# Optimization experiments

Hardware: AMD Instinct MI355X
Metric: run time of the kernel (lower is better)

The kernel has to match this reference:

```python
import jax, jax.numpy as jnp
import numpy as np

H = 256
N = 64           # d_state; diagonal SSM uses N//2 conjugate-pair modes
N2 = N // 2
B, L = 16, 4096
EPS = 1e-5


def layernorm(x, g, b):
    m = jnp.mean(x, axis=-1, keepdims=True)
    v = jnp.mean((x - m) ** 2, axis=-1, keepdims=True)
    return (x - m) / jnp.sqrt(v + EPS) * g + b


def s4_layer(u, log_dt, A_re, A_im, C_re, C_im, D, Wout, bout):
    # u: (B, L, H). Bidirectional diagonal S4 (S4D-style ZOH kernel), channels=1.
    Bb, Ll, Hh = u.shape
    dt = jnp.exp(log_dt)                       # (H,)
    A = A_re + 1j * A_im                       # (H, N2), Re(A) < 0
    dtA = dt[:, None] * A                      # (H, N2)
    # ZOH discretization folded into C:  C <- C * (exp(dtA) - 1) / A
    C = (C_re + 1j * C_im) * (jnp.exp(dtA) - 1.0) / A   # (2, H, N2)
    vand = jnp.exp(dtA[:, :, None] * jnp.arange(Ll))    # (H, N2, L)
    k = 2.0 * jnp.einsum('chn,hnl->chl', C, vand).real  # (2, H, L)
    k_fwd, k_bwd = k[0], k[1]
    # bidirectional: causal kernel + anticausal (flipped, shifted by L)
    z = jnp.zeros_like(k_fwd)
    k2 = jnp.concatenate([k_fwd, z], axis=-1) \
       + jnp.concatenate([z, k_bwd[:, ::-1]], axis=-1)  # (H, 2L)
    ut = jnp.transpose(u, (0, 2, 1))                    # (B, H, L)
    n_fft = 2 * Ll
    y = jnp.fft.irfft(jnp.fft.rfft(ut, n=n_fft) * jnp.fft.rfft(k2, n=n_fft), n=n_fft)[..., :Ll]
    y = y + ut * D[:, None]                             # skip connection
    y = jax.nn.gelu(y, approximate=False)
    y = jnp.transpose(y, (0, 2, 1))                     # (B, L, H)
    zz = y @ Wout + bout                                # (B, L, 2H)
    return zz[..., :Hh] * jax.nn.sigmoid(zz[..., Hh:])  # GLU output projection


def setup_inputs() -> dict:
    key = jax.random.key(0)
    ks = jax.random.split(key, 16)
    x = jax.random.normal(ks[0], (B, L, H), dtype=jnp.float32)
    log_dt = jnp.log(0.001) + jax.random.uniform(ks[1], (H,)) * (jnp.log(0.1) - jnp.log(0.001))
    A_re = -0.5 * jnp.ones((H, N2), dtype=jnp.float32)
    A_im = jnp.pi * jnp.broadcast_to(jnp.arange(N2, dtype=jnp.float32), (H, N2))
    C_re = jax.random.normal(ks[2], (2, H, N2), dtype=jnp.float32) * 0.5
    C_im = jax.random.normal(ks[3], (2, H, N2), dtype=jnp.float32) * 0.5
    Dskip = jax.random.normal(ks[4], (H,), dtype=jnp.float32)
    Wout = jax.random.normal(ks[5], (H, 2 * H), dtype=jnp.float32) / np.sqrt(H)
    bout = jnp.zeros((2 * H,), dtype=jnp.float32)
    ln1_g = jnp.ones((H,), jnp.float32); ln1_b = jnp.zeros((H,), jnp.float32)
    ln2_g = jnp.ones((H,), jnp.float32); ln2_b = jnp.zeros((H,), jnp.float32)
    W2 = jax.random.normal(ks[6], (H, 2 * H), dtype=jnp.float32) / np.sqrt(H)
    b2 = jnp.zeros((2 * H,), jnp.float32)
    W3 = jax.random.normal(ks[7], (2 * H, H), dtype=jnp.float32) / np.sqrt(2 * H)
    b3 = jnp.zeros((H,), jnp.float32)
    return dict(x=x, ln1_g=ln1_g, ln1_b=ln1_b, ln2_g=ln2_g, ln2_b=ln2_b,
                log_dt=log_dt, A_re=A_re, A_im=A_im, C_re=C_re, C_im=C_im,
                Dskip=Dskip, Wout=Wout, bout=bout, W2=W2, b2=b2, W3=W3, b3=b3)


def reference(x, ln1_g, ln1_b, ln2_g, ln2_b, log_dt, A_re, A_im, C_re, C_im,
              Dskip, Wout, bout, W2, b2, W3, b3):
    # residual S4 sub-block
    y = x
    h = layernorm(x, ln1_g, ln1_b)
    h = s4_layer(h, log_dt, A_re, A_im, C_re, C_im, Dskip, Wout, bout)
    x = y + h
    # residual MLP sub-block
    y = x
    h = layernorm(x, ln2_g, ln2_b)
    h = jax.nn.gelu(h @ W2 + b2, approximate=False)
    h = h @ W3 + b3
    return y + h
```

## Files before the change

### kernel.cpp

```cpp
#include <hip/hip_runtime.h>
#include <hip/hip_bf16.h>

typedef __attribute__((ext_vector_type(8))) short bf16x8;
typedef __attribute__((ext_vector_type(4))) float f32x4;

#define Hdim 256
#define NM 32
#define NB 16
#define LL 4096
#define PCH 256
#define NCH 16
#define KBIG 384

#define OFF_ABIG ((size_t)0)
#define OFF_WPM  ((size_t)50331648)
#define OFF_UT   ((size_t)67108864)
#define OFF_ZG   ((size_t)100663296)
#define OFF_M    ((size_t)67108864)
#define OFF_ZP   ((size_t)134217728)
#define OFF_G    ((size_t)150994944)
#define OFF_WTAB ((size_t)185073664)
#define OFF_WPT  ((size_t)185139200)
#define OFF_CE   ((size_t)185204736)
#define OFF_W1T  ((size_t)185335808)
#define OFF_W2T  ((size_t)185597952)
#define OFF_W3T  ((size_t)185860096)

typedef const __attribute__((address_space(1))) void* gas_p;
typedef __attribute__((address_space(3))) void* las_p;

__device__ __forceinline__ float gelu_f(float v) {
    float u = 0.7978845608028654f * fmaf(0.044715f * v * v, v, v);
    float uc = fminf(fmaxf(u, -15.f), 15.f);
    float e = __expf(2.f * uc);
    return 0.5f * v * (1.f + (e - 1.f) * __builtin_amdgcn_rcpf(e + 1.f));
}
__device__ __forceinline__ unsigned short f2bf(float f) {
    unsigned int u = __float_as_uint(f);
    u += 0x7fffu + ((u >> 16) & 1u);
    return (unsigned short)(u >> 16);
}
__device__ __forceinline__ float bf2f(unsigned short u) {
    return __uint_as_float((unsigned int)u << 16);
}

__device__ __forceinline__ bf16x8 fr(const unsigned short* lds, int row, int kcol) {
    return *(const bf16x8*)(lds + row * 64 + ((((kcol >> 3) ^ (row & 7)) << 3)));
}

template<int ROWS, int THREADS>
__device__ __forceinline__ void stage64(const unsigned short* __restrict__ src, int ld, int k0,
                                        unsigned short* lds, int t) {
    constexpr int EPI = THREADS * 8;
#pragma unroll
    for (int i = 0; i < (ROWS * 64) / EPI; i++) {
        int e = i * EPI + t * 8;
        int r = e >> 6;
        int k = (((e >> 3) & 7) ^ (r & 7)) << 3;
        const unsigned short* g = src + (size_t)r * ld + (k0 + k);
        unsigned short* l = lds + i * EPI + (t >> 6) * 512;
        __builtin_amdgcn_global_load_lds((gas_p)g, (las_p)l, 16, 0, 0);
    }
}

template<int ROWS, int THREADS>
__device__ __forceinline__ void stageUT(const unsigned short* __restrict__ UT, int h, int rbase,
                                        int k0, unsigned short* lds, int t) {
    constexpr int EPI = THREADS * 8;
#pragma unroll
    for (int i = 0; i < (ROWS * 64) / EPI; i++) {
        int e = i * EPI + t * 8;
        int r = e >> 6;
        int k = (((e >> 3) & 7) ^ (r & 7)) << 3;
        int row = rbase + r;
        const unsigned short* g = UT + ((size_t)((row >> 4) * Hdim + h)) * LL
                                  + (row & 15) * PCH + (k0 + k);
        unsigned short* l = lds + i * EPI + (t >> 6) * 512;
        __builtin_amdgcn_global_load_lds((gas_p)g, (las_p)l, 16, 0, 0);
    }
}

__global__ void k_tab(const float* __restrict__ logdt, const float* __restrict__ Are,
                      const float* __restrict__ Aim, const float* __restrict__ Cre,
                      const float* __restrict__ Cim, float2* __restrict__ wtab,
                      float2* __restrict__ wptab, float2* __restrict__ ceff) {
    int idx = blockIdx.x * blockDim.x + threadIdx.x;
    if (idx >= Hdim * NM) return;
    int h = idx >> 5;
    float dt = expf(logdt[h]);
    double dar = (double)dt * (double)Are[idx];
    double dai = (double)dt * (double)Aim[idx];
    double wm = exp(dar);
    double wr = wm * cos(dai), wi = wm * sin(dai);
    wtab[idx] = make_float2((float)wr, (float)wi);
    double pm = exp(dar * (double)PCH);
    double pai = dai * (double)PCH;
    wptab[idx] = make_float2((float)(pm * cos(pai)), (float)(pm * sin(pai)));
    double are = (double)Are[idx], aim = (double)Aim[idx];
    double den = are * are + aim * aim;
    double nr = wr - 1.0, ni = wi;
    double qr = (nr * are + ni * aim) / den;
    double qi = (ni * are - nr * aim) / den;
    for (int ch = 0; ch < 2; ch++) {
        double cr = (double)Cre[ch * Hdim * NM + idx];
        double ci = (double)Cim[ch * Hdim * NM + idx];
        ceff[ch * Hdim * NM + idx] = make_float2((float)(cr * qr - ci * qi),
                                                 (float)(cr * qi + ci * qr));
    }
}

__global__ void k_wt(const float* __restrict__ W1, const float* __restrict__ W2,
                     const float* __restrict__ W3, unsigned short* __restrict__ W1T,
                     unsigned short* __restrict__ W2T, unsigned short* __restrict__ W3T) {
    int t = blockIdx.x * 256 + threadIdx.x;
    int k = t >> 9, n = t & 511;
    W1T[n * 256 + k] = f2bf(W1[t]);
    W2T[n * 256 + k] = f2bf(W2[t]);
    int k3 = t >> 8, n3 = t & 255;
    W3T[n3 * 512 + k3] = f2bf(W3[t]);
}

__global__ __launch_bounds__(256) void k_abw(const float* __restrict__ logdt,
                                             const float* __restrict__ Are,
                                             const float* __restrict__ Aim,
                                             const float2* __restrict__ CE,
                                             const float* __restrict__ Dsk,
                                             unsigned short* __restrict__ AB,
                                             unsigned short* __restrict__ Wp) {
    __shared__ float2 wpow[32][257];
    __shared__ float kf[256], kb[256];
    __shared__ float2 ce_s[64];
    int h = blockIdx.x;
    int part = blockIdx.y;
    int t = threadIdx.x;
    if (t < 64) ce_s[t] = CE[(t >> 5) * (Hdim * NM) + h * NM + (t & 31)];
    {
        int n = t >> 3, seg = t & 7;
        float dt = expf(logdt[h]);
        float dar = dt * Are[h * NM + n], dai = dt * Aim[h * NM + n];
        float em = expf(dar);
        float wr = em * cosf(dai), wi = em * sinf(dai);
        int j0 = seg * 32;
        float m = expf((float)j0 * dar), ang = (float)j0 * dai;
        float vr = m * cosf(ang), vi = m * sinf(ang);
        for (int q = 0; q < 32; q++) {
            wpow[n][j0 + q] = make_float2(vr, vi);
            float nr2 = vr * wr - vi * wi;
            float ni2 = vr * wi + vi * wr;
            vr = nr2; vi = ni2;
        }
        if (seg == 7) wpow[n][256] = make_float2(vr, vi);
    }
    __syncthreads();
    if (part == 4) {
        for (int r = 0; r < 128; r++) {
            int n = (r & 63) >> 1, reim = r & 1, dir = r >> 6;
            float2 wv = wpow[n][dir ? t : 255 - t];
            Wp[((size_t)h * 128 + r) * 256 + t] = f2bf(reim ? wv.y : wv.x);
        }
        return;
    }
    {
        float kfv = 0.f, kbv = 0.f;
#pragma unroll
        for (int n = 0; n < NM; n++) {
            float2 wv = wpow[n][t];
            float2 cf = ce_s[n], cb = ce_s[32 + n];
            kfv = fmaf(cf.x, wv.x, fmaf(-cf.y, wv.y, kfv));
            kbv = fmaf(cb.x, wv.x, fmaf(-cb.y, wv.y, kbv));
        }
        kf[t] = 2.f * kfv;
        kb[t] = 2.f * kbv;
    }
    __syncthreads();
    float dsk = Dsk[h];
    int j0 = part * 64;
    for (int j = j0; j < j0 + 64; j++) {
        unsigned short* out = AB + ((size_t)h * 256 + j) * KBIG;
        float v = (t <= j) ? kf[j - t] : kb[t - j - 1];
        if (t == j) v += dsk;
        out[t] = f2bf(v);
        if (t < 128) {
            int n = (t & 63) >> 1, reim = t & 1;
            float2 c = (t < 64) ? ce_s[n] : ce_s[32 + n];
            float2 wv = (t < 64) ? wpow[n][j + 1] : wpow[n][255 - j];
            float re = c.x * wv.x - c.y * wv.y;
            float im = c.x * wv.y + c.y * wv.x;
            out[256 + t] = f2bf(reim ? -2.f * im : 2.f * re);
        }
    }
}

__global__ __launch_bounds__(256) void k_lntr(const float* __restrict__ x,
                                              const float* __restrict__ g,
                                              const float* __restrict__ bt,
                                              unsigned short* __restrict__ UT) {
    __shared__ unsigned short lds[256][65];
    int lt = blockIdx.x, b = blockIdx.y;
    int t = threadIdx.x;
    int lane = t & 63, w = t >> 6;
    float4 gg = ((const float4*)g)[lane];
    float4 bb = ((const float4*)bt)[lane];
#pragma unroll
    for (int q = 0; q < 16; q++) {
        int l = q * 4 + w;
        float4 v = ((const float4*)(x + ((size_t)(b * LL + lt * 64 + l)) * Hdim))[lane];
        float s = v.x + v.y + v.z + v.w;
        float ss = v.x * v.x + v.y * v.y + v.z * v.z + v.w * v.w;
#pragma unroll
        for (int o = 1; o < 64; o <<= 1) { s += __shfl_xor(s, o, 64); ss += __shfl_xor(ss, o, 64); }
        float mean = s * (1.0f / Hdim);
        float var = ss * (1.0f / Hdim) - mean * mean;
        float rstd = rsqrtf(var + 1e-5f);
        lds[lane * 4 + 0][l] = f2bf((v.x - mean) * rstd * gg.x + bb.x);
        lds[lane * 4 + 1][l] = f2bf((v.y - mean) * rstd * gg.y + bb.y);
        lds[lane * 4 + 2][l] = f2bf((v.z - mean) * rstd * gg.z + bb.z);
        lds[lane * 4 + 3][l] = f2bf((v.w - mean) * rstd * gg.w + bb.w);
    }
    __syncthreads();
    for (int q = 0; q < 64; q++) {
        int idx = q * 256 + t;
        int hh = idx >> 6, ll = idx & 63;
        UT[((size_t)(b * Hdim + hh)) * LL + lt * 64 + ll] = lds[hh][ll];
    }
}

__global__ void k_ln_bf(const unsigned short* __restrict__ x, const float* __restrict__ g,
                        const float* __restrict__ bt, unsigned short* __restrict__ out) {
    int row = blockIdx.x * 4 + (threadIdx.x >> 6);
    int lane = threadIdx.x & 63;
    ushort4 u4 = ((const ushort4*)(x + (size_t)row * Hdim))[lane];
    float vx = bf2f(u4.x), vy = bf2f(u4.y), vz = bf2f(u4.z), vw = bf2f(u4.w);
    float s = vx + vy + vz + vw;
    float ss = vx * vx + vy * vy + vz * vz + vw * vw;
#pragma unroll
    for (int o = 1; o < 64; o <<= 1) { s += __shfl_xor(s, o, 64); ss += __shfl_xor(ss, o, 64); }
    float mean = s * (1.0f / Hdim);
    float var = ss * (1.0f / Hdim) - mean * mean;
    float rstd = rsqrtf(var + 1e-5f);
    float4 gg = ((const float4*)g)[lane];
    float4 bb = ((const float4*)bt)[lane];
    ushort4 o;
    o.x = f2bf((vx - mean) * rstd * gg.x + bb.x);
    o.y = f2bf((vy - mean) * rstd * gg.y + bb.y);
    o.z = f2bf((vz - mean) * rstd * gg.z + bb.z);
    o.w = f2bf((vw - mean) * rstd * gg.w + bb.w);
    ((ushort4*)(out + (size_t)row * Hdim))[lane] = o;
}

__global__ __launch_bounds__(512) void k_zgemm(const unsigned short* __restrict__ UT,
                                               const unsigned short* __restrict__ Wp,
                                               float* __restrict__ Zg) {
    __shared__ unsigned short As[256 * 64];
    __shared__ unsigned short Bs[128 * 64];
    int h = blockIdx.x;
    int t = threadIdx.x;
    int w = t >> 6, lane = t & 63;
    int m0 = (w & 3) * 64;
    int nb = (w >> 2) * 64;
    int lr = lane & 15, lk = (lane >> 4) * 8;
    f32x4 acc[4][4];
#pragma unroll
    for (int i = 0; i < 4; i++)
#pragma unroll
        for (int jx = 0; jx < 4; jx++) acc[i][jx] = (f32x4){0.f, 0.f, 0.f, 0.f};
    for (int k0 = 0; k0 < 256; k0 += 64) {
        stageUT<256, 512>(UT, h, 0, k0, As, t);
        stage64<128, 512>(Wp + (size_t)h * 128 * 256, 256, k0, Bs, t);
        __syncthreads();
#pragma unroll
        for (int kk = 0; kk < 64; kk += 32) {
            bf16x8 a[4], b[4];
#pragma unroll
            for (int mi = 0; mi < 4; mi++) a[mi] = fr(As, m0 + mi * 16 + lr, kk + lk);
#pragma unroll
            for (int nf = 0; nf < 4; nf++) b[nf] = fr(Bs, nb + nf * 16 + lr, kk + lk);
#pragma unroll
            for (int mi = 0; mi < 4; mi++)
#pragma unroll
                for (int nf = 0; nf < 4; nf++)
                    acc[mi][nf] = __builtin_amdgcn_mfma_f32_16x16x32_bf16(a[mi], b[nf], acc[mi][nf], 0, 0, 0);
        }
        __syncthreads();
    }
#pragma unroll
    for (int mi = 0; mi < 4; mi++)
#pragma unroll
        for (int nf = 0; nf < 4; nf++) {
            int col = nb + nf * 16 + lr;
#pragma unroll
            for (int r = 0; r < 4; r++) {
                int row = m0 + mi * 16 + (lane >> 4) * 4 + r;
                Zg[((size_t)h * 256 + row) * 128 + col] = acc[mi][nf][r];
            }
        }
}

__global__ void k_prefix2(const float* __restrict__ Zg, const float2* __restrict__ wptab,
                          unsigned short* __restrict__ ZP) {
    int t = blockIdx.x * 256 + threadIdx.x;
    int n = t & 31;
    int h = (t >> 5) & 255;
    int b = (t >> 13) & 15;
    int dir = (t >> 17) & 1;
    float2 wp = wptab[h * NM + n];
    float sr = 0.f, si = 0.f;
    int ro = dir ? 64 + 2 * n : 2 * n;
    if (dir == 0) {
        for (int c = 0; c < NCH; c++) {
            size_t base = ((size_t)h * 256 + b * NCH + c) * 128;
            ZP[base + ro] = f2bf(sr);
            ZP[base + ro + 1] = f2bf(si);
            float zr = Zg[base + ro], zi = Zg[base + ro + 1];
            float nr = fmaf(wp.x, sr, fmaf(-wp.y, si, zr));
            float ni = fmaf(wp.y, sr, fmaf(wp.x, si, zi));
            sr = nr; si = ni;
        }
    } else {
        for (int c = NCH - 1; c >= 0; c--) {
            size_t base = ((size_t)h * 256 + b * NCH + c) * 128;
            ZP[base + ro] = f2bf(sr);
            ZP[base + ro + 1] = f2bf(si);
            float zr = Zg[base + ro], zi = Zg[base + ro + 1];
            float nr = fmaf(wp.x, sr, fmaf(-wp.y, si, zr));
            float ni = fmaf(wp.y, sr, fmaf(wp.x, si, zi));
            sr = nr; si = ni;
        }
    }
}

__global__ __launch_bounds__(512) void k_conv(const unsigned short* __restrict__ UT,
                                              const unsigned short* __restrict__ ZP,
                                              const unsigned short* __restrict__ AB,
                                              unsigned short* __restrict__ Yt) {
    __shared__ unsigned short As[128 * 64];
    __shared__ unsigned short Bs[256 * 64];
    int wgid = ((int)blockIdx.x % 8) * 64 + (int)blockIdx.x / 8;
    int h = wgid >> 1;
    int mbase = (wgid & 1) * 128;
    int t = threadIdx.x;
    int w = t >> 6, lane = t & 63;
    int m0 = (w & 1) * 64;
    int nb = (w >> 1) * 64;
    int lr = lane & 15, lk = (lane >> 4) * 8;
    const unsigned short* ABh = AB + (size_t)h * 256 * KBIG;
    f32x4 acc[4][4];
#pragma unroll
    for (int i = 0; i < 4; i++)
#pragma unroll
        for (int jx = 0; jx < 4; jx++) acc[i][jx] = (f32x4){0.f, 0.f, 0.f, 0.f};
    for (int k0 = 0; k0 < 256; k0 += 64) {
        stageUT<128, 512>(UT, h, mbase, k0, As, t);
        stage64<256, 512>(ABh, KBIG, k0, Bs, t);
        __syncthreads();
#pragma unroll
        for (int kk = 0; kk < 64; kk += 32) {
            bf16x8 a[4], b[4];
#pragma unroll
            for (int mi = 0; mi < 4; mi++) a[mi] = fr(As, m0 + mi * 16 + lr, kk + lk);
#pragma unroll
            for (int nf = 0; nf < 4; nf++) b[nf] = fr(Bs, nb + nf * 16 + lr, kk + lk);
#pragma unroll
            for (int mi = 0; mi < 4; mi++)
#pragma unroll
                for (int nf = 0; nf < 4; nf++)
                    acc[mi][nf] = __builtin_amdgcn_mfma_f32_16x16x32_bf16(a[mi], b[nf], acc[mi][nf], 0, 0, 0);
        }
        __syncthreads();
    }
    for (int k0 = 0; k0 < 128; k0 += 64) {
        stage64<128, 512>(ZP + ((size_t)h * 256 + mbase) * 128, 128, k0, As, t);
        stage64<256, 512>(ABh + 256, KBIG, k0, Bs, t);
        __syncthreads();
#pragma unroll
        for (int kk = 0; kk < 64; kk += 32) {
            bf16x8 a[4], b[4];
#pragma unroll
            for (int mi = 0; mi < 4; mi++) a[mi] = fr(As, m0 + mi * 16 + lr, kk + lk);
#pragma unroll
            for (int nf = 0; nf < 4; nf++) b[nf] = fr(Bs, nb + nf * 16 + lr, kk + lk);
#pragma unroll
            for (int mi = 0; mi < 4; mi++)
#pragma unroll
                for (int nf = 0; nf < 4; nf++)
                    acc[mi][nf] = __builtin_amdgcn_mfma_f32_16x16x32_bf16(a[mi], b[nf], acc[mi][nf], 0, 0, 0);
        }
        __syncthreads();
    }
#pragma unroll
    for (int mi = 0; mi < 4; mi++)
#pragma unroll
        for (int nf = 0; nf < 4; nf++) {
            int col = nb + nf * 16 + lr;
#pragma unroll
            for (int r = 0; r < 4; r++) {
                int row = mbase + m0 + mi * 16 + (lane >> 4) * 4 + r;
                Yt[(size_t)h * 65536 + row * 256 + col] = f2bf(gelu_f(acc[mi][nf][r]));
            }
        }
}

__global__ void k_trg(const unsigned short* __restrict__ Yt, unsigned short* __restrict__ G) {
    __shared__ unsigned short lds[64][65];
    int bc = blockIdx.x;
    int h0 = blockIdx.y * 64, j0 = blockIdx.z * 64;
    int t = threadIdx.x;
#pragma unroll
    for (int q = 0; q < 16; q++) {
        int idx = q * 256 + t;
        int hh = idx >> 6, jj = idx & 63;
        lds[hh][jj] = Yt[(size_t)(h0 + hh) * 65536 + bc * 256 + j0 + jj];
    }
    __syncthreads();
    int b = bc >> 4, c = bc & 15;
#pragma unroll
    for (int q = 0; q < 16; q++) {
        int idx = q * 256 + t;
        int jj = idx >> 6, hh = idx & 63;
        G[((size_t)(b * LL + c * PCH + j0 + jj)) * Hdim + h0 + hh] = lds[hh][jj];
    }
}

__global__ __launch_bounds__(512) void k_gemm1(const unsigned short* __restrict__ Gm,
                                               const unsigned short* __restrict__ W1T,
                                               const float* __restrict__ bo,
                                               const float* __restrict__ xin,
                                               unsigned short* __restrict__ X2) {
    __shared__ unsigned short As[128 * 64];
    __shared__ unsigned short BsA[128 * 64];
    __shared__ unsigned short BsB[128 * 64];
    int t = threadIdx.x;
    int w = t >> 6, lane = t & 63;
    int m0w = (w & 1) * 64;
    int n0w = (w >> 1) * 32;
    int lr = lane & 15, lk = (lane >> 4) * 8;
    int mblk = blockIdx.x * 128, nblk = blockIdx.y * 128;
    const unsigned short* Ab  = Gm + (size_t)mblk * 256;
    const unsigned short* BbA = W1T + (size_t)nblk * 256;
    const unsigned short* BbB = W1T + (size_t)(nblk + 256) * 256;
    f32x4 acc[4][4];
#pragma unroll
    for (int i = 0; i < 4; i++)
#pragma unroll
        for (int j = 0; j < 4; j++) acc[i][j] = (f32x4){0.f, 0.f, 0.f, 0.f};
    for (int k0 = 0; k0 < 256; k0 += 64) {
        stage64<128, 512>(Ab, 256, k0, As, t);
        stage64<128, 512>(BbA, 256, k0, BsA, t);
        stage64<128, 512>(BbB, 256, k0, BsB, t);
        __syncthreads();
#pragma unroll
        for (int kk = 0; kk < 64; kk += 32) {
            bf16x8 a[4], bA[2], bB[2];
#pragma unroll
            for (int mi = 0; mi < 4; mi++)
                a[mi] = fr(As, m0w + mi * 16 + lr, kk + lk);
#pragma unroll
            for (int nf = 0; nf < 2; nf++) {
                bA[nf] = fr(BsA, n0w + nf * 16 + lr, kk + lk);
                bB[nf] = fr(BsB, n0w + nf * 16 + lr, kk + lk);
            }
#pragma unroll
            for (int mi = 0; mi < 4; mi++)
#pragma unroll
                for (int nf = 0; nf < 2; nf++) {
                    acc[mi][nf] = __builtin_amdgcn_mfma_f32_16x16x32_bf16(a[mi], bA[nf], acc[mi][nf], 0, 0, 0);
                    acc[mi][nf + 2] = __builtin_amdgcn_mfma_f32_16x16x32_bf16(a[mi], bB[nf], acc[mi][nf + 2], 0, 0, 0);
                }
        }
        __syncthreads();
    }
#pragma unroll
    for (int mi = 0; mi < 4; mi++)
#pragma unroll
        for (int nf = 0; nf < 2; nf++) {
            int col = nblk + n0w + nf * 16 + lr;
            float biasA = bo[col], biasB = bo[col + 256];
#pragma unroll
            for (int r = 0; r < 4; r++) {
                int row = mblk + m0w + mi * 16 + (lane >> 4) * 4 + r;
                float zzA = acc[mi][nf][r] + biasA;
                float zzB = acc[mi][nf + 2][r] + biasB;
                float v = zzA * __builtin_amdgcn_rcpf(1.0f + __expf(-zzB));
                size_t idx = (size_t)row * 256 + col;
                X2[idx] = f2bf(xin[idx] + v);
            }
        }
}

__global__ __launch_bounds__(512) void k_gemm2(const unsigned short* __restrict__ T2,
                                               const unsigned short* __restrict__ W2T,
                                               const float* __restrict__ b2,
                                               unsigned short* __restrict__ Mo) {
    __shared__ unsigned short As[128 * 64];
    __shared__ unsigned short Bs[256 * 64];
    int t = threadIdx.x;
    int w = t >> 6, lane = t & 63;
    int m0w = (w & 1) * 64;
    int n0w = (w >> 1) * 64;
    int lr = lane & 15, lk = (lane >> 4) * 8;
    int mblk = blockIdx.x * 128, nblk = blockIdx.y * 256;
    const unsigned short* Ab = T2 + (size_t)mblk * 256;
    const unsigned short* Bb = W2T + (size_t)nblk * 256;
    f32x4 acc[4][4];
#pragma unroll
    for (int i = 0; i < 4; i++)
#pragma unroll
        for (int j = 0; j < 4; j++) acc[i][j] = (f32x4){0.f, 0.f, 0.f, 0.f};
    for (int k0 = 0; k0 < 256; k0 += 64) {
        stage64<128, 512>(Ab, 256, k0, As, t);
        stage64<256, 512>(Bb, 256, k0, Bs, t);
        __syncthreads();
#pragma unroll
        for (int kk = 0; kk < 64; kk += 32) {
            bf16x8 a[4], b[4];
#pragma unroll
            for (int mi = 0; mi < 4; mi++)
                a[mi] = fr(As, m0w + mi * 16 + lr, kk + lk);
#pragma unroll
            for (int nf = 0; nf < 4; nf++)
                b[nf] = fr(Bs, n0w + nf * 16 + lr, kk + lk);
#pragma unroll
            for (int mi = 0; mi < 4; mi++)
#pragma unroll
                for (int nf = 0; nf < 4; nf++)
                    acc[mi][nf] = __builtin_amdgcn_mfma_f32_16x16x32_bf16(a[mi], b[nf], acc[mi][nf], 0, 0, 0);
        }
        __syncthreads();
    }
#pragma unroll
    for (int mi = 0; mi < 4; mi++)
#pragma unroll
        for (int nf = 0; nf < 4; nf++) {
            int col = nblk + n0w + nf * 16 + lr;
            float bias = b2[col];
#pragma unroll
            for (int r = 0; r < 4; r++) {
                int row = mblk + m0w + mi * 16 + (lane >> 4) * 4 + r;
                Mo[(size_t)row * 512 + col] = f2bf(gelu_f(acc[mi][nf][r] + bias));
            }
        }
}

__global__ __launch_bounds__(512) void k_gemm3(const unsigned short* __restrict__ Mb,
                                               const unsigned short* __restrict__ W3T,
                                               const float* __restrict__ b3,
                                               const unsigned short* __restrict__ X2,
                                               float* __restrict__ out) {
    __shared__ unsigned short As[128 * 64];
    __shared__ unsigned short Bs[256 * 64];
    int t = threadIdx.x;
    int w = t >> 6, lane = t & 63;
    int m0w = (w & 1) * 64;
    int n0w = (w >> 1) * 64;
    int lr = lane & 15, lk = (lane >> 4) * 8;
    int mblk = blockIdx.x * 128;
    const unsigned short* Ab = Mb + (size_t)mblk * 512;
    f32x4 acc[4][4];
#pragma unroll
    for (int i = 0; i < 4; i++)
#pragma unroll
        for (int j = 0; j < 4; j++) acc[i][j] = (f32x4){0.f, 0.f, 0.f, 0.f};
    for (int k0 = 0; k0 < 512; k0 += 64) {
        stage64<128, 512>(Ab, 512, k0, As, t);
        stage64<256, 512>(W3T, 512, k0, Bs, t);
        __syncthreads();
#pragma unroll
        for (int kk = 0; kk < 64; kk += 32) {
            bf16x8 a[4], b[4];
#pragma unroll
            for (int mi = 0; mi < 4; mi++)
                a[mi] = fr(As, m0w + mi * 16 + lr, kk + lk);
#pragma unroll
            for (int nf = 0; nf < 4; nf++)
                b[nf] = fr(Bs, n0w + nf * 16 + lr, kk + lk);
#pragma unroll
            for (int mi = 0; mi < 4; mi++)
#pragma unroll
                for (int nf = 0; nf < 4; nf++)
                    acc[mi][nf] = __builtin_amdgcn_mfma_f32_16x16x32_bf16(a[mi], b[nf], acc[mi][nf], 0, 0, 0);
        }
        __syncthreads();
    }
#pragma unroll
    for (int mi = 0; mi < 4; mi++)
#pragma unroll
        for (int nf = 0; nf < 4; nf++) {
            int col = n0w + nf * 16 + lr;
            float bias = b3[col];
#pragma unroll
            for (int r = 0; r < 4; r++) {
                int row = mblk + m0w + mi * 16 + (lane >> 4) * 4 + r;
                size_t idx = (size_t)row * 256 + col;
                out[idx] = bf2f(X2[idx]) + acc[mi][nf][r] + bias;
            }
        }
}

extern "C" void kernel_launch(void* const* d_in, const int* in_sizes, int n_in,
                              void* d_out, int out_size, void* d_ws, size_t ws_size,
                              hipStream_t stream) {
    const float* x     = (const float*)d_in[0];
    const float* ln1g  = (const float*)d_in[1];
    const float* ln1b  = (const float*)d_in[2];
    const float* ln2g  = (const float*)d_in[3];
    const float* ln2b  = (const float*)d_in[4];
    const float* logdt = (const float*)d_in[5];
    const float* Are   = (const float*)d_in[6];
    const float* Aim   = (const float*)d_in[7];
    const float* Cre   = (const float*)d_in[8];
    const float* Cim   = (const float*)d_in[9];
    const float* Dsk   = (const float*)d_in[10];
    const float* Wout  = (const float*)d_in[11];
    const float* bo    = (const float*)d_in[12];
    const float* W2    = (const float*)d_in[13];
    const float* b2    = (const float*)d_in[14];
    const float* W3    = (const float*)d_in[15];
    const float* b3    = (const float*)d_in[16];

    char* ws = (char*)d_ws;
    unsigned short* AB   = (unsigned short*)(ws + OFF_ABIG);
    unsigned short* Wp   = (unsigned short*)(ws + OFF_WPM);
    unsigned short* X2   = (unsigned short*)(ws + OFF_ABIG);
    unsigned short* UT   = (unsigned short*)(ws + OFF_UT);
    float*          Zg   = (float*)(ws + OFF_ZG);
    unsigned short* Yt   = (unsigned short*)(ws + OFF_ZG);
    unsigned short* Mb   = (unsigned short*)(ws + OFF_M);
    unsigned short* ZP   = (unsigned short*)(ws + OFF_ZP);
    unsigned short* G    = (unsigned short*)(ws + OFF_G);
    float2*         WT   = (float2*)(ws + OFF_WTAB);
    float2*         WPT  = (float2*)(ws + OFF_WPT);
    float2*         CE   = (float2*)(ws + OFF_CE);
    unsigned short* W1T  = (unsigned short*)(ws + OFF_W1T);
    unsigned short* W2T  = (unsigned short*)(ws + OFF_W2T);
    unsigned short* W3T  = (unsigned short*)(ws + OFF_W3T);

    k_tab<<<32, 256, 0, stream>>>(logdt, Are, Aim, Cre, Cim, WT, WPT, CE);
    k_wt<<<512, 256, 0, stream>>>(Wout, W2, W3, W1T, W2T, W3T);
    k_lntr<<<dim3(64, 16), 256, 0, stream>>>(x, ln1g, ln1b, UT);
    k_abw<<<dim3(256, 5), 256, 0, stream>>>(logdt, Are, Aim, CE, Dsk, AB, Wp);
    k_zgemm<<<256, 512, 0, stream>>>(UT, Wp, Zg);
    k_prefix2<<<1024, 256, 0, stream>>>(Zg, WPT, ZP);
    k_conv<<<512, 512, 0, stream>>>(UT, ZP, AB, Yt);
    k_trg<<<dim3(256, 4, 4), 256, 0, stream>>>(Yt, G);
    k_gemm1<<<dim3(512, 2), 512, 0, stream>>>(G, W1T, bo, x, X2);
    k_ln_bf<<<NB * LL / 4, 256, 0, stream>>>(X2, ln2g, ln2b, G);
    k_gemm2<<<dim3(512, 2), 512, 0, stream>>>(G, W2T, b2, Mb);
    k_gemm3<<<512, 512, 0, stream>>>(Mb, W3T, b3, X2, (float*)d_out);
}
```

Before: 254.1 us.

## Build Toeplitz conv tile on the fly from kernel vector instead of materializing

Instead of writing a full 256x256 bf16 Toeplitz matrix (plus D skip) per channel to global memory and reading it back in the conv GEMM, k_abw now writes only a 512-float concatenated kernel vector and a separate state-projection Q matrix. k_conv loads that vector into LDS and builds the swizzled B tiles directly from it, adding D on the diagonal. The wpow table is now filled with interleaved strides, and the Wp and Q outputs are split across the grid's parts so the work is more even. This removes tens of MB of global writes and reads, at the cost of extra per-element LDS reads and bf16 conversions inside the conv kernel's staging.

```diff
diff --git a/kernel.cpp b/kernel.cpp
--- a/kernel.cpp
+++ b/kernel.cpp
@@ -10,9 +10,9 @@
 #define LL 4096
 #define PCH 256
 #define NCH 16
-#define KBIG 384
-
-#define OFF_ABIG ((size_t)0)
+
+#define OFF_Q    ((size_t)0)
+#define OFF_KC   ((size_t)16777216)
 #define OFF_WPM  ((size_t)50331648)
 #define OFF_UT   ((size_t)67108864)
 #define OFF_ZG   ((size_t)100663296)
@@ -124,11 +124,10 @@
                                              const float* __restrict__ Are,
                                              const float* __restrict__ Aim,
                                              const float2* __restrict__ CE,
-                                             const float* __restrict__ Dsk,
-                                             unsigned short* __restrict__ AB,
-                                             unsigned short* __restrict__ Wp) {
-    __shared__ float2 wpow[32][257];
-    __shared__ float kf[256], kb[256];
+                                             unsigned short* __restrict__ Q,
+                                             unsigned short* __restrict__ Wp,
+                                             float* __restrict__ Kcat) {
+    __shared__ float2 wpow[32][258];
     __shared__ float2 ce_s[64];
     int h = blockIdx.x;
     int part = blockIdx.y;
@@ -140,27 +139,21 @@
         float dar = dt * Are[h * NM + n], dai = dt * Aim[h * NM + n];
         float em = expf(dar);
         float wr = em * cosf(dai), wi = em * sinf(dai);
-        int j0 = seg * 32;
-        float m = expf((float)j0 * dar), ang = (float)j0 * dai;
+        float ar = wr, ai = wi;
+#pragma unroll
+        for (int s = 0; s < 3; s++) { float nr = ar * ar - ai * ai, ni = 2.f * ar * ai; ar = nr; ai = ni; }
+        float m = expf((float)seg * dar), ang = (float)seg * dai;
         float vr = m * cosf(ang), vi = m * sinf(ang);
         for (int q = 0; q < 32; q++) {
-            wpow[n][j0 + q] = make_float2(vr, vi);
-            float nr2 = vr * wr - vi * wi;
-            float ni2 = vr * wi + vi * wr;
+            wpow[n][seg + 8 * q] = make_float2(vr, vi);
+            float nr2 = vr * ar - vi * ai;
+            float ni2 = vr * ai + vi * ar;
             vr = nr2; vi = ni2;
         }
-        if (seg == 7) wpow[n][256] = make_float2(vr, vi);
+        if (seg == 0) wpow[n][256] = make_float2(vr, vi);
     }
     __syncthreads();
     if (part == 4) {
-        for (int r = 0; r < 128; r++) {
-            int n = (r & 63) >> 1, reim = r & 1, dir = r >> 6;
-            float2 wv = wpow[n][dir ? t : 255 - t];
-            Wp[((size_t)h * 128 + r) * 256 + t] = f2bf(reim ? wv.y : wv.x);
-        }
-        return;
-    }
-    {
         float kfv = 0.f, kbv = 0.f;
 #pragma unroll
         for (int n = 0; n < NM; n++) {
@@ -169,25 +162,26 @@
             kfv = fmaf(cf.x, wv.x, fmaf(-cf.y, wv.y, kfv));
             kbv = fmaf(cb.x, wv.x, fmaf(-cb.y, wv.y, kbv));
         }
-        kf[t] = 2.f * kfv;
-        kb[t] = 2.f * kbv;
-    }
-    __syncthreads();
-    float dsk = Dsk[h];
-    int j0 = part * 64;
-    for (int j = j0; j < j0 + 64; j++) {
-        unsigned short* out = AB + ((size_t)h * 256 + j) * KBIG;
-        float v = (t <= j) ? kf[j - t] : kb[t - j - 1];
-        if (t == j) v += dsk;
-        out[t] = f2bf(v);
-        if (t < 128) {
-            int n = (t & 63) >> 1, reim = t & 1;
-            float2 c = (t < 64) ? ce_s[n] : ce_s[32 + n];
-            float2 wv = (t < 64) ? wpow[n][j + 1] : wpow[n][255 - j];
-            float re = c.x * wv.x - c.y * wv.y;
-            float im = c.x * wv.y + c.y * wv.x;
-            out[256 + t] = f2bf(reim ? -2.f * im : 2.f * re);
-        }
+        Kcat[(size_t)h * 512 + 255 + t] = 2.f * kfv;
+        if (t < 255) Kcat[(size_t)h * 512 + 254 - t] = 2.f * kbv;
+        if (t == 255) Kcat[(size_t)h * 512 + 511] = 0.f;
+        return;
+    }
+    for (int jj = 0; jj < 32; jj++) {
+        int j = part * 64 + jj * 2 + (t >> 7);
+        int tq = t & 127;
+        int n = (tq & 63) >> 1, reim = tq & 1;
+        float2 c = (tq < 64) ? ce_s[n] : ce_s[32 + n];
+        float2 wv = (tq < 64) ? wpow[n][j + 1] : wpow[n][255 - j];
+        float re = c.x * wv.x - c.y * wv.y;
+        float im = c.x * wv.y + c.y * wv.x;
+        Q[((size_t)h * 256 + j) * 128 + tq] = f2bf(reim ? -2.f * im : 2.f * re);
+    }
+    for (int rr = 0; rr < 32; rr++) {
+        int r = part * 32 + rr;
+        int n = (r & 63) >> 1, reim = r & 1, dir = r >> 6;
+        float2 wv = wpow[n][dir ? t : 255 - t];
+        Wp[((size_t)h * 128 + r) * 256 + t] = f2bf(reim ? wv.y : wv.x);
     }
 }
 
@@ -331,10 +325,13 @@
 
 __global__ __launch_bounds__(512) void k_conv(const unsigned short* __restrict__ UT,
                                               const unsigned short* __restrict__ ZP,
-                                              const unsigned short* __restrict__ AB,
+                                              const unsigned short* __restrict__ Q,
+                                              const float* __restrict__ Kcat,
+                                              const float* __restrict__ Dsk,
                                               unsigned short* __restrict__ Yt) {
     __shared__ unsigned short As[128 * 64];
     __shared__ unsigned short Bs[256 * 64];
+    __shared__ float kcs[512];
     int wgid = ((int)blockIdx.x % 8) * 64 + (int)blockIdx.x / 8;
     int h = wgid >> 1;
     int mbase = (wgid & 1) * 128;
@@ -343,7 +340,9 @@
     int m0 = (w & 1) * 64;
     int nb = (w >> 1) * 64;
     int lr = lane & 15, lk = (lane >> 4) * 8;
-    const unsigned short* ABh = AB + (size_t)h * 256 * KBIG;
+    float dsk = Dsk[h];
+    kcs[t] = Kcat[(size_t)h * 512 + t];
+    __syncthreads();
     f32x4 acc[4][4];
 #pragma unroll
     for (int i = 0; i < 4; i++)
@@ -351,7 +350,21 @@
         for (int jx = 0; jx < 4; jx++) acc[i][jx] = (f32x4){0.f, 0.f, 0.f, 0.f};
     for (int k0 = 0; k0 < 256; k0 += 64) {
         stageUT<128, 512>(UT, h, mbase, k0, As, t);
-        stage64<256, 512>(ABh, KBIG, k0, Bs, t);
+#pragma unroll
+        for (int gq = 0; gq < 4; gq++) {
+            int e = gq * 4096 + t * 8;
+            int j = e >> 6;
+            int i0 = k0 + (e & 63);
+            union { bf16x8 v; unsigned short u[8]; } pk;
+#pragma unroll
+            for (int q = 0; q < 8; q++) {
+                int i = i0 + q;
+                float f = kcs[255 + j - i];
+                if (i == j) f += dsk;
+                pk.u[q] = f2bf(f);
+            }
+            *(bf16x8*)(Bs + j * 64 + (((((e & 63) >> 3)) ^ (j & 7)) << 3)) = pk.v;
+        }
         __syncthreads();
 #pragma unroll
         for (int kk = 0; kk < 64; kk += 32) {
@@ -370,7 +383,7 @@
     }
     for (int k0 = 0; k0 < 128; k0 += 64) {
         stage64<128, 512>(ZP + ((size_t)h * 256 + mbase) * 128, 128, k0, As, t);
-        stage64<256, 512>(ABh + 256, KBIG, k0, Bs, t);
+        stage64<256, 512>(Q + (size_t)h * 256 * 128, 128, k0, Bs, t);
         __syncthreads();
 #pragma unroll
         for (int kk = 0; kk < 64; kk += 32) {
@@ -618,9 +631,10 @@
     const float* b3    = (const float*)d_in[16];
 
     char* ws = (char*)d_ws;
-    unsigned short* AB   = (unsigned short*)(ws + OFF_ABIG);
+    unsigned short* Q    = (unsigned short*)(ws + OFF_Q);
+    float*          Kc   = (float*)(ws + OFF_KC);
     unsigned short* Wp   = (unsigned short*)(ws + OFF_WPM);
-    unsigned short* X2   = (unsigned short*)(ws + OFF_ABIG);
+    unsigned short* X2   = (unsigned short*)(ws + OFF_Q);
     unsigned short* UT   = (unsigned short*)(ws + OFF_UT);
     float*          Zg   = (float*)(ws + OFF_ZG);
     unsigned short* Yt   = (unsigned short*)(ws + OFF_ZG);
@@ -637,10 +651,10 @@
     k_tab<<<32, 256, 0, stream>>>(logdt, Are, Aim, Cre, Cim, WT, WPT, CE);
     k_wt<<<512, 256, 0, stream>>>(Wout, W2, W3, W1T, W2T, W3T);
     k_lntr<<<dim3(64, 16), 256, 0, stream>>>(x, ln1g, ln1b, UT);
-    k_abw<<<dim3(256, 5), 256, 0, stream>>>(logdt, Are, Aim, CE, Dsk, AB, Wp);
+    k_abw<<<dim3(256, 5), 256, 0, stream>>>(logdt, Are, Aim, CE, Q, Wp, Kc);
     k_zgemm<<<256, 512, 0, stream>>>(UT, Wp, Zg);
     k_prefix2<<<1024, 256, 0, stream>>>(Zg, WPT, ZP);
-    k_conv<<<512, 512, 0, stream>>>(UT, ZP, AB, Yt);
+    k_conv<<<512, 512, 0, stream>>>(UT, ZP, Q, Kc, Dsk, Yt);
     k_trg<<<dim3(256, 4, 4), 256, 0, stream>>>(Yt, G);
     k_gemm1<<<dim3(512, 2), 512, 0, stream>>>(G, W1T, bo, x, X2);
     k_ln_bf<<<NB * LL / 4, 256, 0, stream>>>(X2, ln2g, ln2b, G);
```

After: 238.9 us. 6.0% less time.
